# Kernel tuning notes

Measured on AMD Instinct MI355X. Metric: run time of the kernel, lower is better.

The kernel has to match this reference:

```python
import jax, jax.numpy as jnp
import numpy as np

N = 100000
NEG_SLOPE = 0.2
EPS = 1e-16


def _gatconv(h_in, src, dst, W, a_src, a_dst, b):
    # h_in: [N, Fin]; src/dst: [E_tot] (self-loops included); W: [Fin, Fout]
    h = h_in @ W                                  # [N, Fout]
    alpha_s = h @ a_src                           # [N]
    alpha_d = h @ a_dst                           # [N]
    e = alpha_s[src] + alpha_d[dst]               # [E_tot]
    e = jnp.where(e > 0, e, NEG_SLOPE * e)        # leaky_relu
    m = jax.ops.segment_max(e, dst, num_segments=N)
    e = jnp.exp(e - m[dst])
    s = jax.ops.segment_sum(e, dst, num_segments=N)
    alpha = e / (s[dst] + EPS)                    # segment softmax over in-edges of each dst
    out = jax.ops.segment_sum(alpha[:, None] * h[src], dst, num_segments=N)
    return out + b


def setup_inputs() -> dict:
    key = jax.random.key(0)
    ks = jax.random.split(key, 10)
    Fin, Fh, Fo = 64, 64, 40
    E = 1600000
    x = jax.random.normal(ks[0], (N, Fin), dtype=jnp.float32)
    edge_index = jax.random.randint(ks[1], (2, E), 0, N, dtype=jnp.int64)
    g = 1.0 / np.sqrt(Fin)
    W1 = jax.random.uniform(ks[2], (Fin, Fh), jnp.float32, -g, g)
    a_src1 = jax.random.uniform(ks[3], (Fh,), jnp.float32, -g, g)
    a_dst1 = jax.random.uniform(ks[4], (Fh,), jnp.float32, -g, g)
    b1 = jnp.zeros((Fh,), jnp.float32)
    g2 = 1.0 / np.sqrt(Fh)
    W2 = jax.random.uniform(ks[5], (Fh, Fo), jnp.float32, -g2, g2)
    a_src2 = jax.random.uniform(ks[6], (Fo,), jnp.float32, -g2, g2)
    a_dst2 = jax.random.uniform(ks[7], (Fo,), jnp.float32, -g2, g2)
    b2 = jnp.zeros((Fo,), jnp.float32)
    return {"x": x, "edge_index": edge_index, "W1": W1, "a_src1": a_src1,
            "a_dst1": a_dst1, "b1": b1, "W2": W2, "a_src2": a_src2,
            "a_dst2": a_dst2, "b2": b2}


def reference(x, edge_index, W1, a_src1, a_dst1, b1, W2, a_src2, a_dst2, b2):
    # add self loops (PyG GATConv default)
    loops = jnp.arange(N, dtype=edge_index.dtype)
    src = jnp.concatenate([edge_index[0], loops])
    dst = jnp.concatenate([edge_index[1], loops])
    h = _gatconv(x, src, dst, W1, a_src1, a_dst1, b1)
    h = jax.nn.relu(h)  # dropout p=0 / eval -> no-op
    h = _gatconv(h, src, dst, W2, a_src2, a_dst2, b2)
    return jax.nn.log_softmax(h, axis=-1)
```

## Files before the change

### kernel.cpp

```cpp
#include <hip/hip_runtime.h>
#include <math.h>

#ifndef NEG_SLOPE
#define NEG_SLOPE 0.2f
#endif

#define BUCK_BITS 9
#define BUCK_SIZE 512
#define BUCK_CAP  12288
#define PA_ILP    8

__global__ void detect_i64(const int* __restrict__ ei, int* __restrict__ flag) {
    int lane = threadIdx.x & 63;
    int bad = 0;
    for (int j = 0; j < 4; ++j) bad |= (ei[2 * (lane * 4 + j) + 1] != 0);
    unsigned long long m = __ballot(bad);
    if (lane == 0) *flag = (m == 0ull) ? 1 : 0;
}

__device__ __forceinline__ void get_edge(const void* ei, int is64, int e, int E,
                                         int& s, int& d) {
    if (e >= E) { s = e - E; d = s; return; }
    if (is64) {
        const long long* p = (const long long*)ei;
        s = (int)p[e];
        d = (int)p[(long long)E + e];
    } else {
        const int* p = (const int*)ei;
        s = p[e];
        d = p[E + e];
    }
}

__device__ __forceinline__ unsigned f2bf1(float x) {
    unsigned u = __float_as_uint(x);
    return (u + 0x7fffu + ((u >> 16) & 1u)) >> 16;
}

template <int F, int TPR>
__global__ __launch_bounds__(256) void gemm_att(
    const float* __restrict__ A, const float* __restrict__ W,
    const float* __restrict__ avs, const float* __restrict__ avd,
    unsigned short* __restrict__ Hb, float* __restrict__ as_out,
    float* __restrict__ ad_out, int Nrows) {
    constexpr int K = 64;
    constexpr int R = 256 / TPR;
    constexpr int C = F / TPR;
    __shared__ float sW[K * F];
    __shared__ float sA[R * (K + 4)];
    __shared__ float sas[F], sad[F];

    const int t = threadIdx.x;
    for (int i = t; i < K * F / 4; i += 256)
        ((float4*)sW)[i] = ((const float4*)W)[i];
    for (int i = t; i < F; i += 256) { sas[i] = avs[i]; sad[i] = avd[i]; }

    const int base = blockIdx.x * R;
    for (int i = t; i < R * (K / 4); i += 256) {
        int row = i >> 4;
        int c4  = i & 15;
        float4 v = make_float4(0.f, 0.f, 0.f, 0.f);
        if (base + row < Nrows)
            v = ((const float4*)(A + (size_t)(base + row) * K))[c4];
        float* dp = &sA[row * (K + 4) + c4 * 4];
        dp[0] = v.x; dp[1] = v.y; dp[2] = v.z; dp[3] = v.w;
    }
    __syncthreads();

    const int r  = t / TPR;
    const int f0 = (t % TPR) * C;
    float acc[C];
#pragma unroll
    for (int j = 0; j < C; ++j) acc[j] = 0.f;
    const float* sa = &sA[r * (K + 4)];
#pragma unroll
    for (int k = 0; k < K; ++k) {
        float av = sa[k];
        const float* w = &sW[k * F + f0];
#pragma unroll
        for (int j = 0; j < C; ++j) acc[j] += av * w[j];
    }

    float ps = 0.f, pd = 0.f;
#pragma unroll
    for (int j = 0; j < C; ++j) { ps += acc[j] * sas[f0 + j]; pd += acc[j] * sad[f0 + j]; }
#pragma unroll
    for (int off = 1; off < TPR; off <<= 1) {
        ps += __shfl_xor(ps, off);
        pd += __shfl_xor(pd, off);
    }

    const int row = base + r;
    if (row < Nrows) {
        if ((t % TPR) == 0) { as_out[row] = ps; ad_out[row] = pd; }
        unsigned* hp = (unsigned*)(Hb + (size_t)row * F + f0);
#pragma unroll
        for (int j = 0; j < C / 2; ++j)
            hp[j] = f2bf1(acc[2 * j]) | (f2bf1(acc[2 * j + 1]) << 16);
    }
}

__global__ __launch_bounds__(256) void bucket_bin(
    const void* __restrict__ ei, const int* __restrict__ flag,
    int* __restrict__ fill, int2* __restrict__ pairs, int E, int Etot) {
    __shared__ int cnt[256];
    __shared__ int goff[256];
    const int is64 = *flag;
    const int t = threadIdx.x;
    cnt[t] = 0;
    __syncthreads();
    const int base = blockIdx.x * (256 * PA_ILP) + t;
    int s[PA_ILP], d[PA_ILP], r[PA_ILP];
    bool ok[PA_ILP];
#pragma unroll
    for (int u = 0; u < PA_ILP; ++u) {
        int e = base + u * 256;
        ok[u] = (e < Etot);
        s[u] = d[u] = 0;
        if (ok[u]) get_edge(ei, is64, e, E, s[u], d[u]);
    }
#pragma unroll
    for (int u = 0; u < PA_ILP; ++u)
        if (ok[u]) r[u] = atomicAdd(&cnt[d[u] >> BUCK_BITS], 1);
    __syncthreads();
    if (cnt[t] > 0) goff[t] = atomicAdd(&fill[t], cnt[t]);
    __syncthreads();
#pragma unroll
    for (int u = 0; u < PA_ILP; ++u) {
        if (ok[u]) {
            int b = d[u] >> BUCK_BITS;
            int idx = goff[b] + r[u];
            if (idx < BUCK_CAP)
                pairs[(size_t)b * BUCK_CAP + idx] = make_int2(s[u], d[u]);
        }
    }
}

__global__ void bucket_scan(const int* __restrict__ fill, int* __restrict__ bases,
                            int* __restrict__ row_ptrN, int nbuck) {
    const int lane = threadIdx.x & 63;
    int v[4];
    int loc = 0;
#pragma unroll
    for (int i = 0; i < 4; ++i) {
        int idx = lane * 4 + i;
        v[i] = (idx < nbuck) ? fill[idx] : 0;
        loc += v[i];
    }
    int x = loc;
    for (int off = 1; off < 64; off <<= 1) {
        int y = __shfl_up(x, off);
        if (lane >= off) x += y;
    }
    int run = x - loc;
#pragma unroll
    for (int i = 0; i < 4; ++i) {
        int idx = lane * 4 + i;
        if (idx < nbuck) bases[idx] = run;
        run += v[i];
    }
    if (lane == 63) *row_ptrN = x;
}

__global__ __launch_bounds__(256) void bucket_csr(
    const int2* __restrict__ pairs, const int* __restrict__ fill,
    const int* __restrict__ bases, int* __restrict__ row_ptr,
    int* __restrict__ csr_src, int N) {
    __shared__ int cnt[BUCK_SIZE];
    __shared__ int offs[BUCK_SIZE];
    const int b = blockIdx.x;
    const int base_d = b << BUCK_BITS;
    const int t = threadIdx.x;
    int m = fill[b];
    if (m > BUCK_CAP) m = BUCK_CAP;
    const int gb = bases[b];
    cnt[t] = 0; cnt[t + 256] = 0;
    __syncthreads();
    const int2* bp = pairs + (size_t)b * BUCK_CAP;

    int i = t;
    for (; i + 768 < m; i += 1024) {
        int2 p0 = bp[i], p1 = bp[i + 256], p2 = bp[i + 512], p3 = bp[i + 768];
        atomicAdd(&cnt[p0.y - base_d], 1);
        atomicAdd(&cnt[p1.y - base_d], 1);
        atomicAdd(&cnt[p2.y - base_d], 1);
        atomicAdd(&cnt[p3.y - base_d], 1);
    }
    for (; i < m; i += 256) atomicAdd(&cnt[bp[i].y - base_d], 1);
    __syncthreads();

    if (t < 64) {
        int v[8];
        int loc = 0;
#pragma unroll
        for (int j = 0; j < 8; ++j) { v[j] = cnt[t * 8 + j]; loc += v[j]; }
        int x = loc;
        for (int off = 1; off < 64; off <<= 1) {
            int y = __shfl_up(x, off);
            if (t >= off) x += y;
        }
        int run = x - loc;
#pragma unroll
        for (int j = 0; j < 8; ++j) { offs[t * 8 + j] = gb + run; run += v[j]; }
    }
    __syncthreads();

    for (int k = t; k < BUCK_SIZE; k += 256) {
        int d = base_d + k;
        if (d < N) row_ptr[d] = offs[k];
    }
    __syncthreads();

    i = t;
    for (; i + 768 < m; i += 1024) {
        int2 p0 = bp[i], p1 = bp[i + 256], p2 = bp[i + 512], p3 = bp[i + 768];
        csr_src[atomicAdd(&offs[p0.y - base_d], 1)] = p0.x;
        csr_src[atomicAdd(&offs[p1.y - base_d], 1)] = p1.x;
        csr_src[atomicAdd(&offs[p2.y - base_d], 1)] = p2.x;
        csr_src[atomicAdd(&offs[p3.y - base_d], 1)] = p3.x;
    }
    for (; i < m; i += 256) {
        int2 p = bp[i];
        csr_src[atomicAdd(&offs[p.y - base_d], 1)] = p.x;
    }
}

__device__ __forceinline__ void bf16x8_fma(uint4 hv, float w, float* acc) {
    const unsigned* u = (const unsigned*)&hv;
#pragma unroll
    for (int i = 0; i < 4; ++i) {
        float lo = __uint_as_float(u[i] << 16);
        float hi = __uint_as_float(u[i] & 0xffff0000u);
        acc[2 * i]     += w * lo;
        acc[2 * i + 1] += w * hi;
    }
}

template <int F, int NC, bool RELU, bool LSM>
__global__ __launch_bounds__(256) void gat_aggregate4(
    const int* __restrict__ row_ptr, const int* __restrict__ csr_src,
    const float* __restrict__ asn, const float* __restrict__ adn,
    const unsigned short* __restrict__ Hb, const float* __restrict__ bias,
    float* __restrict__ out, int N) {
    const int lane    = threadIdx.x & 63;
    const int sub     = lane & 15;
    const int half    = sub >> 3;
    const int q       = sub & 7;
    const int grpbase = lane & 48;
    const int node    = blockIdx.x * 16 + (threadIdx.x >> 4);
    const bool valid  = node < N;
    const int nd      = valid ? node : N - 1;
    const int qc      = (q < NC) ? q : NC - 1;
    const float qmask = (q < NC) ? 1.f : 0.f;

    const int r0 = row_ptr[nd], r1 = row_ptr[nd + 1];
    const float add = adn[nd];

    float acc[8];
#pragma unroll
    for (int i = 0; i < 8; ++i) acc[i] = 0.f;
    float Ssum = 0.f;

    for (int base = r0; base < r1; base += 16) {
        int cnt = r1 - base;
        if (cnt > 16) cnt = 16;
        int s = 0;
        float w = 0.f;
        if (sub < cnt) {
            s = csr_src[base + sub];
            float v = asn[s] + add;
            v = v > 0.f ? v : NEG_SLOPE * v;
            w = __expf(v);
        }
        Ssum += w;
        for (int j = 0; j < cnt; j += 8) {
            int se[4]; float we[4]; uint4 hv[4];
#pragma unroll
            for (int k = 0; k < 4; ++k) {
                int e = j + 2 * k + half;
                int src_lane = grpbase | (e & 15);
                se[k] = __shfl(s, src_lane);
                float wk = __shfl(w, src_lane) * qmask;
                we[k] = (e < cnt) ? wk : 0.f;
            }
#pragma unroll
            for (int k = 0; k < 4; ++k)
                hv[k] = *(const uint4*)(Hb + (size_t)se[k] * F + qc * 8);
#pragma unroll
            for (int k = 0; k < 4; ++k) bf16x8_fma(hv[k], we[k], acc);
        }
    }
#pragma unroll
    for (int i = 0; i < 8; ++i) acc[i] += __shfl_xor(acc[i], 8);
#pragma unroll
    for (int off = 1; off < 16; off <<= 1) Ssum += __shfl_xor(Ssum, off);
    const float inv = 1.f / (Ssum + 1e-16f);
    float r[8];
#pragma unroll
    for (int i = 0; i < 8; ++i) r[i] = acc[i] * inv;

    if (LSM) {
        float val[8];
#pragma unroll
        for (int i = 0; i < 8; ++i) val[i] = r[i] + bias[qc * 8 + i];
        float mx = -3.0e38f;
        if (q < NC) {
#pragma unroll
            for (int i = 0; i < 8; ++i) mx = fmaxf(mx, val[i]);
        }
#pragma unroll
        for (int off = 1; off <= 4; off <<= 1) mx = fmaxf(mx, __shfl_xor(mx, off));
        float sm = 0.f;
        if (q < NC) {
#pragma unroll
            for (int i = 0; i < 8; ++i) sm += __expf(val[i] - mx);
        }
#pragma unroll
        for (int off = 1; off <= 4; off <<= 1) sm += __shfl_xor(sm, off);
        float ls = logf(sm) + mx;
        if (valid && half == 0 && q < NC) {
            float* op = out + (size_t)node * F + q * 8;
            ((float4*)op)[0] = make_float4(val[0] - ls, val[1] - ls, val[2] - ls, val[3] - ls);
            ((float4*)op)[1] = make_float4(val[4] - ls, val[5] - ls, val[6] - ls, val[7] - ls);
        }
    } else {
        if (valid && half == 0 && q < NC) {
            float* op = out + (size_t)node * F + q * 8;
            float4 o0, o1;
            o0.x = r[0] + bias[q * 8 + 0]; o0.y = r[1] + bias[q * 8 + 1];
            o0.z = r[2] + bias[q * 8 + 2]; o0.w = r[3] + bias[q * 8 + 3];
            o1.x = r[4] + bias[q * 8 + 4]; o1.y = r[5] + bias[q * 8 + 5];
            o1.z = r[6] + bias[q * 8 + 6]; o1.w = r[7] + bias[q * 8 + 7];
            if (RELU) {
                o0.x = fmaxf(o0.x, 0.f); o0.y = fmaxf(o0.y, 0.f);
                o0.z = fmaxf(o0.z, 0.f); o0.w = fmaxf(o0.w, 0.f);
                o1.x = fmaxf(o1.x, 0.f); o1.y = fmaxf(o1.y, 0.f);
                o1.z = fmaxf(o1.z, 0.f); o1.w = fmaxf(o1.w, 0.f);
            }
            ((float4*)op)[0] = o0;
            ((float4*)op)[1] = o1;
        }
    }
}

extern "C" void kernel_launch(void* const* d_in, const int* in_sizes, int n_in,
                              void* d_out, int out_size, void* d_ws, size_t ws_size,
                              hipStream_t stream) {
    const float* x   = (const float*)d_in[0];
    const void*  ei  = d_in[1];
    const float* W1  = (const float*)d_in[2];
    const float* as1 = (const float*)d_in[3];
    const float* ad1 = (const float*)d_in[4];
    const float* b1  = (const float*)d_in[5];
    const float* W2  = (const float*)d_in[6];
    const float* as2 = (const float*)d_in[7];
    const float* ad2 = (const float*)d_in[8];
    const float* b2  = (const float*)d_in[9];
    float* out = (float*)d_out;

    const int N     = in_sizes[0] / 64;
    const int E     = in_sizes[1] / 2;
    const int Etot  = E + N;
    const int nbuck = (N + BUCK_SIZE - 1) >> BUCK_BITS;

    float* ws = (float*)d_ws;
    unsigned short* hb = (unsigned short*)ws;  ws += (size_t)N * 32;
    float* agg1 = ws;              ws += (size_t)N * 64;
    float* asn  = ws;              ws += N;
    float* adn  = ws;              ws += N;
    int* row_ptr = (int*)ws;       ws += N + 1;
    int* csr_src = (int*)ws;       ws += Etot;
    int* fill   = (int*)ws;        ws += 256;
    int* bases  = (int*)ws;        ws += 256;
    int* flag   = (int*)ws;
    int2* pairs = (int2*)hb;

    detect_i64<<<1, 64, 0, stream>>>((const int*)ei, flag);

    hipMemsetAsync(fill, 0, 256 * sizeof(int), stream);
    {
        int pb = (Etot + 256 * PA_ILP - 1) / (256 * PA_ILP);
        bucket_bin<<<pb, 256, 0, stream>>>(ei, flag, fill, pairs, E, Etot);
    }
    bucket_scan<<<1, 64, 0, stream>>>(fill, bases, &row_ptr[N], nbuck);
    bucket_csr<<<nbuck, 256, 0, stream>>>(pairs, fill, bases, row_ptr, csr_src, N);

    const int AGG_B = (N + 15) / 16;

    gemm_att<64, 4><<<(N + 63) / 64, 256, 0, stream>>>(x, W1, as1, ad1, hb, asn, adn, N);
    gat_aggregate4<64, 8, true, false><<<AGG_B, 256, 0, stream>>>(
        row_ptr, csr_src, asn, adn, hb, b1, agg1, N);

    gemm_att<40, 4><<<(N + 63) / 64, 256, 0, stream>>>(agg1, W2, as2, ad2, hb, asn, adn, N);
    gat_aggregate4<40, 5, false, true><<<AGG_B, 256, 0, stream>>>(
        row_ptr, csr_src, asn, adn, hb, b2, out, N);
}
```

Before: 263.4 us.

## Fuse edge binning with layer-1 GEMM and layer-1 aggregation with layer-2 GEMM

Merges the i64 detection, edge bucketing and the first dense projection into one heterogeneous launch, with blocks split by index. The bucket prefix scan moves into each bucket_csr block. The layer-1 softmax aggregation is fused with the layer-2 projection and attention dot products, so the fp32 hidden activations are never written to or reread from global memory. This cuts launch count and a large intermediate round trip, at the cost of heavier shared-memory use, lower occupancy in the fused kernels, and a separate pairs buffer that enlarges the workspace.

```diff
diff --git a/kernel.cpp b/kernel.cpp
--- a/kernel.cpp
+++ b/kernel.cpp
@@ -9,14 +9,6 @@
 #define BUCK_SIZE 512
 #define BUCK_CAP  12288
 #define PA_ILP    8
-
-__global__ void detect_i64(const int* __restrict__ ei, int* __restrict__ flag) {
-    int lane = threadIdx.x & 63;
-    int bad = 0;
-    for (int j = 0; j < 4; ++j) bad |= (ei[2 * (lane * 4 + j) + 1] != 0);
-    unsigned long long m = __ballot(bad);
-    if (lane == 0) *flag = (m == 0ull) ? 1 : 0;
-}
 
 __device__ __forceinline__ void get_edge(const void* ei, int is64, int e, int E,
                                          int& s, int& d) {
@@ -37,145 +29,150 @@
     return (u + 0x7fffu + ((u >> 16) & 1u)) >> 16;
 }
 
-template <int F, int TPR>
-__global__ __launch_bounds__(256) void gemm_att(
-    const float* __restrict__ A, const float* __restrict__ W,
+__global__ __launch_bounds__(256) void bin_gemm1(
+    const void* __restrict__ ei, int E, int Etot, int binB,
+    int* __restrict__ fill, int2* __restrict__ pairs,
+    const float* __restrict__ x, const float* __restrict__ W1,
     const float* __restrict__ avs, const float* __restrict__ avd,
-    unsigned short* __restrict__ Hb, float* __restrict__ as_out,
-    float* __restrict__ ad_out, int Nrows) {
-    constexpr int K = 64;
-    constexpr int R = 256 / TPR;
-    constexpr int C = F / TPR;
-    __shared__ float sW[K * F];
-    __shared__ float sA[R * (K + 4)];
-    __shared__ float sas[F], sad[F];
-
+    unsigned short* __restrict__ Hb, float* __restrict__ asn,
+    float* __restrict__ adn, int N) {
+    __shared__ __align__(16) char smem[34816];
     const int t = threadIdx.x;
-    for (int i = t; i < K * F / 4; i += 256)
-        ((float4*)sW)[i] = ((const float4*)W)[i];
-    for (int i = t; i < F; i += 256) { sas[i] = avs[i]; sad[i] = avd[i]; }
-
-    const int base = blockIdx.x * R;
-    for (int i = t; i < R * (K / 4); i += 256) {
-        int row = i >> 4;
-        int c4  = i & 15;
-        float4 v = make_float4(0.f, 0.f, 0.f, 0.f);
-        if (base + row < Nrows)
-            v = ((const float4*)(A + (size_t)(base + row) * K))[c4];
-        float* dp = &sA[row * (K + 4) + c4 * 4];
-        dp[0] = v.x; dp[1] = v.y; dp[2] = v.z; dp[3] = v.w;
-    }
-    __syncthreads();
-
-    const int r  = t / TPR;
-    const int f0 = (t % TPR) * C;
-    float acc[C];
-#pragma unroll
-    for (int j = 0; j < C; ++j) acc[j] = 0.f;
-    const float* sa = &sA[r * (K + 4)];
-#pragma unroll
-    for (int k = 0; k < K; ++k) {
-        float av = sa[k];
-        const float* w = &sW[k * F + f0];
-#pragma unroll
-        for (int j = 0; j < C; ++j) acc[j] += av * w[j];
-    }
-
-    float ps = 0.f, pd = 0.f;
-#pragma unroll
-    for (int j = 0; j < C; ++j) { ps += acc[j] * sas[f0 + j]; pd += acc[j] * sad[f0 + j]; }
-#pragma unroll
-    for (int off = 1; off < TPR; off <<= 1) {
-        ps += __shfl_xor(ps, off);
-        pd += __shfl_xor(pd, off);
-    }
-
-    const int row = base + r;
-    if (row < Nrows) {
-        if ((t % TPR) == 0) { as_out[row] = ps; ad_out[row] = pd; }
-        unsigned* hp = (unsigned*)(Hb + (size_t)row * F + f0);
-#pragma unroll
-        for (int j = 0; j < C / 2; ++j)
-            hp[j] = f2bf1(acc[2 * j]) | (f2bf1(acc[2 * j + 1]) << 16);
-    }
-}
-
-__global__ __launch_bounds__(256) void bucket_bin(
-    const void* __restrict__ ei, const int* __restrict__ flag,
-    int* __restrict__ fill, int2* __restrict__ pairs, int E, int Etot) {
-    __shared__ int cnt[256];
-    __shared__ int goff[256];
-    const int is64 = *flag;
-    const int t = threadIdx.x;
-    cnt[t] = 0;
-    __syncthreads();
-    const int base = blockIdx.x * (256 * PA_ILP) + t;
-    int s[PA_ILP], d[PA_ILP], r[PA_ILP];
-    bool ok[PA_ILP];
-#pragma unroll
-    for (int u = 0; u < PA_ILP; ++u) {
-        int e = base + u * 256;
-        ok[u] = (e < Etot);
-        s[u] = d[u] = 0;
-        if (ok[u]) get_edge(ei, is64, e, E, s[u], d[u]);
-    }
-#pragma unroll
-    for (int u = 0; u < PA_ILP; ++u)
-        if (ok[u]) r[u] = atomicAdd(&cnt[d[u] >> BUCK_BITS], 1);
-    __syncthreads();
-    if (cnt[t] > 0) goff[t] = atomicAdd(&fill[t], cnt[t]);
-    __syncthreads();
-#pragma unroll
-    for (int u = 0; u < PA_ILP; ++u) {
-        if (ok[u]) {
-            int b = d[u] >> BUCK_BITS;
-            int idx = goff[b] + r[u];
-            if (idx < BUCK_CAP)
-                pairs[(size_t)b * BUCK_CAP + idx] = make_int2(s[u], d[u]);
-        }
-    }
-}
-
-__global__ void bucket_scan(const int* __restrict__ fill, int* __restrict__ bases,
-                            int* __restrict__ row_ptrN, int nbuck) {
-    const int lane = threadIdx.x & 63;
-    int v[4];
-    int loc = 0;
-#pragma unroll
-    for (int i = 0; i < 4; ++i) {
-        int idx = lane * 4 + i;
-        v[i] = (idx < nbuck) ? fill[idx] : 0;
-        loc += v[i];
-    }
-    int x = loc;
-    for (int off = 1; off < 64; off <<= 1) {
-        int y = __shfl_up(x, off);
-        if (lane >= off) x += y;
-    }
-    int run = x - loc;
-#pragma unroll
-    for (int i = 0; i < 4; ++i) {
-        int idx = lane * 4 + i;
-        if (idx < nbuck) bases[idx] = run;
-        run += v[i];
-    }
-    if (lane == 63) *row_ptrN = x;
+
+    if ((int)blockIdx.x < binB) {
+        int* cnt   = (int*)smem;
+        int* goff  = cnt + 256;
+        int* sflag = goff + 256;
+        if (t < 64) {
+            const int* p = (const int*)ei;
+            int bad = 0;
+            for (int j = 0; j < 4; ++j) bad |= (p[2 * (t * 4 + j) + 1] != 0);
+            unsigned long long m = __ballot(bad);
+            if (t == 0) *sflag = (m == 0ull) ? 1 : 0;
+        }
+        cnt[t] = 0;
+        __syncthreads();
+        const int is64 = *sflag;
+        const int base = blockIdx.x * (256 * PA_ILP) + t;
+        int s[PA_ILP], d[PA_ILP], r[PA_ILP];
+        bool ok[PA_ILP];
+#pragma unroll
+        for (int u = 0; u < PA_ILP; ++u) {
+            int e = base + u * 256;
+            ok[u] = (e < Etot);
+            s[u] = d[u] = 0;
+            if (ok[u]) get_edge(ei, is64, e, E, s[u], d[u]);
+        }
+#pragma unroll
+        for (int u = 0; u < PA_ILP; ++u)
+            if (ok[u]) r[u] = atomicAdd(&cnt[d[u] >> BUCK_BITS], 1);
+        __syncthreads();
+        if (cnt[t] > 0) goff[t] = atomicAdd(&fill[t], cnt[t]);
+        __syncthreads();
+#pragma unroll
+        for (int u = 0; u < PA_ILP; ++u) {
+            if (ok[u]) {
+                int b = d[u] >> BUCK_BITS;
+                int idx = goff[b] + r[u];
+                if (idx < BUCK_CAP)
+                    pairs[(size_t)b * BUCK_CAP + idx] = make_int2(s[u], d[u]);
+            }
+        }
+    } else {
+        constexpr int K = 64, F = 64, TPR = 4, R = 64, C = 16;
+        float* sW  = (float*)smem;
+        float* sA  = sW + K * F;
+        float* sas = sA + R * (K + 4);
+        float* sad = sas + F;
+
+        for (int i = t; i < K * F / 4; i += 256)
+            ((float4*)sW)[i] = ((const float4*)W1)[i];
+        for (int i = t; i < F; i += 256) { sas[i] = avs[i]; sad[i] = avd[i]; }
+
+        const int base = (blockIdx.x - binB) * R;
+        for (int i = t; i < R * (K / 4); i += 256) {
+            int row = i >> 4;
+            int c4  = i & 15;
+            float4 v = make_float4(0.f, 0.f, 0.f, 0.f);
+            if (base + row < N)
+                v = ((const float4*)(x + (size_t)(base + row) * K))[c4];
+            float* dp = &sA[row * (K + 4) + c4 * 4];
+            dp[0] = v.x; dp[1] = v.y; dp[2] = v.z; dp[3] = v.w;
+        }
+        __syncthreads();
+
+        const int r  = t / TPR;
+        const int f0 = (t % TPR) * C;
+        float acc[C];
+#pragma unroll
+        for (int j = 0; j < C; ++j) acc[j] = 0.f;
+        const float* sa = &sA[r * (K + 4)];
+#pragma unroll
+        for (int k = 0; k < K; ++k) {
+            float av = sa[k];
+            const float* w = &sW[k * F + f0];
+#pragma unroll
+            for (int j = 0; j < C; ++j) acc[j] += av * w[j];
+        }
+        float ps = 0.f, pd = 0.f;
+#pragma unroll
+        for (int j = 0; j < C; ++j) { ps += acc[j] * sas[f0 + j]; pd += acc[j] * sad[f0 + j]; }
+#pragma unroll
+        for (int off = 1; off < TPR; off <<= 1) {
+            ps += __shfl_xor(ps, off);
+            pd += __shfl_xor(pd, off);
+        }
+        const int row = base + r;
+        if (row < N) {
+            if ((t % TPR) == 0) { asn[row] = ps; adn[row] = pd; }
+            unsigned* hp = (unsigned*)(Hb + (size_t)row * F + f0);
+#pragma unroll
+            for (int j = 0; j < C / 2; ++j)
+                hp[j] = f2bf1(acc[2 * j]) | (f2bf1(acc[2 * j + 1]) << 16);
+        }
+    }
 }
 
 __global__ __launch_bounds__(256) void bucket_csr(
     const int2* __restrict__ pairs, const int* __restrict__ fill,
-    const int* __restrict__ bases, int* __restrict__ row_ptr,
-    int* __restrict__ csr_src, int N) {
+    int* __restrict__ row_ptr, int* __restrict__ csr_src, int N, int nbuck) {
     __shared__ int cnt[BUCK_SIZE];
     __shared__ int offs[BUCK_SIZE];
+    __shared__ int sbase[256];
+    __shared__ int stot;
+    const int t = threadIdx.x;
+    if (t < 64) {
+        int v[4];
+        int loc = 0;
+#pragma unroll
+        for (int i = 0; i < 4; ++i) {
+            int idx = t * 4 + i;
+            v[i] = (idx < nbuck) ? fill[idx] : 0;
+            loc += v[i];
+        }
+        int x = loc;
+        for (int off = 1; off < 64; off <<= 1) {
+            int y = __shfl_up(x, off);
+            if (t >= off) x += y;
+        }
+        int run = x - loc;
+#pragma unroll
+        for (int i = 0; i < 4; ++i) {
+            int idx = t * 4 + i;
+            if (idx < 256) sbase[idx] = run;
+            run += v[i];
+        }
+        if (t == 63) stot = x;
+    }
+    cnt[t] = 0; cnt[t + 256] = 0;
+    __syncthreads();
+
     const int b = blockIdx.x;
     const int base_d = b << BUCK_BITS;
-    const int t = threadIdx.x;
+    const int gb = sbase[b];
     int m = fill[b];
     if (m > BUCK_CAP) m = BUCK_CAP;
-    const int gb = bases[b];
-    cnt[t] = 0; cnt[t + 256] = 0;
-    __syncthreads();
+    if (b == 0 && t == 0) row_ptr[N] = stot;
     const int2* bp = pairs + (size_t)b * BUCK_CAP;
 
     int i = t;
@@ -236,12 +233,115 @@
     }
 }
 
-template <int F, int NC, bool RELU, bool LSM>
-__global__ __launch_bounds__(256) void gat_aggregate4(
+__global__ __launch_bounds__(256) void agg1_gemm2(
+    const int* __restrict__ row_ptr, const int* __restrict__ csr_src,
+    const float* __restrict__ asn1, const float* __restrict__ adn1,
+    const unsigned short* __restrict__ Hb, const float* __restrict__ b1,
+    const float* __restrict__ W2, const float* __restrict__ a_s2,
+    const float* __restrict__ a_d2, unsigned short* __restrict__ Hb2,
+    float* __restrict__ asn2, float* __restrict__ adn2, int N) {
+    __shared__ float sW2[64 * 40];
+    __shared__ float sa2[40], sd2[40], sb1[64];
+    __shared__ float rowbuf[16][68];
+    const int t = threadIdx.x;
+    for (int i = t; i < 640; i += 256) ((float4*)sW2)[i] = ((const float4*)W2)[i];
+    if (t < 40) { sa2[t] = a_s2[t]; sd2[t] = a_d2[t]; }
+    if (t >= 64 && t < 128) sb1[t - 64] = b1[t - 64];
+    __syncthreads();
+
+    const int lane    = t & 63;
+    const int sub     = lane & 15;
+    const int half    = sub >> 3;
+    const int q       = sub & 7;
+    const int grpbase = lane & 48;
+    const int slot    = t >> 4;
+    const int node    = blockIdx.x * 16 + slot;
+    const bool valid  = node < N;
+    const int nd      = valid ? node : N - 1;
+
+    const int r0 = row_ptr[nd], r1 = row_ptr[nd + 1];
+    const float add = adn1[nd];
+
+    float acc[8];
+#pragma unroll
+    for (int i = 0; i < 8; ++i) acc[i] = 0.f;
+    float Ssum = 0.f;
+
+    for (int base = r0; base < r1; base += 16) {
+        int cnt = r1 - base;
+        if (cnt > 16) cnt = 16;
+        int s = 0;
+        float w = 0.f;
+        if (sub < cnt) {
+            s = csr_src[base + sub];
+            float v = asn1[s] + add;
+            v = v > 0.f ? v : NEG_SLOPE * v;
+            w = __expf(v);
+        }
+        Ssum += w;
+        for (int j = 0; j < cnt; j += 8) {
+            int se[4]; float we[4]; uint4 hv[4];
+#pragma unroll
+            for (int k = 0; k < 4; ++k) {
+                int e = j + 2 * k + half;
+                int src_lane = grpbase | (e & 15);
+                se[k] = __shfl(s, src_lane);
+                float wk = __shfl(w, src_lane);
+                we[k] = (e < cnt) ? wk : 0.f;
+            }
+#pragma unroll
+            for (int k = 0; k < 4; ++k)
+                hv[k] = *(const uint4*)(Hb + (size_t)se[k] * 64 + q * 8);
+#pragma unroll
+            for (int k = 0; k < 4; ++k) bf16x8_fma(hv[k], we[k], acc);
+        }
+    }
+#pragma unroll
+    for (int i = 0; i < 8; ++i) acc[i] += __shfl_xor(acc[i], 8);
+#pragma unroll
+    for (int off = 1; off < 16; off <<= 1) Ssum += __shfl_xor(Ssum, off);
+    const float inv = 1.f / (Ssum + 1e-16f);
+
+    float row[8];
+#pragma unroll
+    for (int i = 0; i < 8; ++i) row[i] = fmaxf(acc[i] * inv + sb1[q * 8 + i], 0.f);
+    if (half == 0) {
+#pragma unroll
+        for (int i = 0; i < 8; ++i) rowbuf[slot][q * 8 + i] = row[i];
+    }
+
+    const bool m2 = (sub + 32) < 40;
+    const int f2c = m2 ? sub + 32 : 39;
+    float h2a = 0.f, h2b = 0.f, h2c = 0.f;
+#pragma unroll 8
+    for (int k = 0; k < 64; ++k) {
+        float a = rowbuf[slot][k];
+        h2a += a * sW2[k * 40 + sub];
+        h2b += a * sW2[k * 40 + sub + 16];
+        h2c += a * sW2[k * 40 + f2c];
+    }
+    float ps = h2a * sa2[sub] + h2b * sa2[sub + 16] + (m2 ? h2c * sa2[sub + 32] : 0.f);
+    float pd = h2a * sd2[sub] + h2b * sd2[sub + 16] + (m2 ? h2c * sd2[sub + 32] : 0.f);
+#pragma unroll
+    for (int off = 1; off < 16; off <<= 1) {
+        ps += __shfl_xor(ps, off);
+        pd += __shfl_xor(pd, off);
+    }
+    if (valid) {
+        unsigned short* hp = Hb2 + (size_t)node * 40;
+        hp[sub]      = (unsigned short)f2bf1(h2a);
+        hp[sub + 16] = (unsigned short)f2bf1(h2b);
+        if (m2) hp[sub + 32] = (unsigned short)f2bf1(h2c);
+        if (sub == 0) { asn2[node] = ps; adn2[node] = pd; }
+    }
+}
+
+__global__ __launch_bounds__(256) void agg2_lsm(
     const int* __restrict__ row_ptr, const int* __restrict__ csr_src,
     const float* __restrict__ asn, const float* __restrict__ adn,
     const unsigned short* __restrict__ Hb, const float* __restrict__ bias,
     float* __restrict__ out, int N) {
+    constexpr int F = 40, NC = 5;
     const int lane    = threadIdx.x & 63;
     const int sub     = lane & 15;
     const int half    = sub >> 3;
@@ -299,47 +399,28 @@
 #pragma unroll
     for (int i = 0; i < 8; ++i) r[i] = acc[i] * inv;
 
-    if (LSM) {
-        float val[8];
-#pragma unroll
-        for (int i = 0; i < 8; ++i) val[i] = r[i] + bias[qc * 8 + i];
-        float mx = -3.0e38f;
-        if (q < NC) {
-#pragma unroll
-            for (int i = 0; i < 8; ++i) mx = fmaxf(mx, val[i]);
-        }
-#pragma unroll
-        for (int off = 1; off <= 4; off <<= 1) mx = fmaxf(mx, __shfl_xor(mx, off));
-        float sm = 0.f;
-        if (q < NC) {
-#pragma unroll
-            for (int i = 0; i < 8; ++i) sm += __expf(val[i] - mx);
-        }
-#pragma unroll
-        for (int off = 1; off <= 4; off <<= 1) sm += __shfl_xor(sm, off);
-        float ls = logf(sm) + mx;
-        if (valid && half == 0 && q < NC) {
-            float* op = out + (size_t)node * F + q * 8;
-            ((float4*)op)[0] = make_float4(val[0] - ls, val[1] - ls, val[2] - ls, val[3] - ls);
-            ((float4*)op)[1] = make_float4(val[4] - ls, val[5] - ls, val[6] - ls, val[7] - ls);
-        }
-    } else {
-        if (valid && half == 0 && q < NC) {
-            float* op = out + (size_t)node * F + q * 8;
-            float4 o0, o1;
-            o0.x = r[0] + bias[q * 8 + 0]; o0.y = r[1] + bias[q * 8 + 1];
-            o0.z = r[2] + bias[q * 8 + 2]; o0.w = r[3] + bias[q * 8 + 3];
-            o1.x = r[4] + bias[q * 8 + 4]; o1.y = r[5] + bias[q * 8 + 5];
-            o1.z = r[6] + bias[q * 8 + 6]; o1.w = r[7] + bias[q * 8 + 7];
-            if (RELU) {
-                o0.x = fmaxf(o0.x, 0.f); o0.y = fmaxf(o0.y, 0.f);
-                o0.z = fmaxf(o0.z, 0.f); o0.w = fmaxf(o0.w, 0.f);
-                o1.x = fmaxf(o1.x, 0.f); o1.y = fmaxf(o1.y, 0.f);
-                o1.z = fmaxf(o1.z, 0.f); o1.w = fmaxf(o1.w, 0.f);
-            }
-            ((float4*)op)[0] = o0;
-            ((float4*)op)[1] = o1;
-        }
+    float val[8];
+#pragma unroll
+    for (int i = 0; i < 8; ++i) val[i] = r[i] + bias[qc * 8 + i];
+    float mx = -3.0e38f;
+    if (q < NC) {
+#pragma unroll
+        for (int i = 0; i < 8; ++i) mx = fmaxf(mx, val[i]);
+    }
+#pragma unroll
+    for (int off = 1; off <= 4; off <<= 1) mx = fmaxf(mx, __shfl_xor(mx, off));
+    float sm = 0.f;
+    if (q < NC) {
+#pragma unroll
+        for (int i = 0; i < 8; ++i) sm += __expf(val[i] - mx);
+    }
+#pragma unroll
+    for (int off = 1; off <= 4; off <<= 1) sm += __shfl_xor(sm, off);
+    float ls = logf(sm) + mx;
+    if (valid && half == 0 && q < NC) {
+        float* op = out + (size_t)node * F + q * 8;
+        ((float4*)op)[0] = make_float4(val[0] - ls, val[1] - ls, val[2] - ls, val[3] - ls);
+        ((float4*)op)[1] = make_float4(val[4] - ls, val[5] - ls, val[6] - ls, val[7] - ls);
     }
 }
 
@@ -364,34 +445,27 @@
     const int nbuck = (N + BUCK_SIZE - 1) >> BUCK_BITS;
 
     float* ws = (float*)d_ws;
-    unsigned short* hb = (unsigned short*)ws;  ws += (size_t)N * 32;
-    float* agg1 = ws;              ws += (size_t)N * 64;
-    float* asn  = ws;              ws += N;
-    float* adn  = ws;              ws += N;
+    unsigned short* hb  = (unsigned short*)ws;  ws += (size_t)N * 32;
+    unsigned short* hb2 = (unsigned short*)ws;  ws += (size_t)N * 20;
+    float* asn1 = ws;              ws += N;
+    float* adn1 = ws;              ws += N;
+    float* asn2 = ws;              ws += N;
+    float* adn2 = ws;              ws += N;
     int* row_ptr = (int*)ws;       ws += N + 1;
     int* csr_src = (int*)ws;       ws += Etot;
     int* fill   = (int*)ws;        ws += 256;
-    int* bases  = (int*)ws;        ws += 256;
-    int* flag   = (int*)ws;
-    int2* pairs = (int2*)hb;
-
-    detect_i64<<<1, 64, 0, stream>>>((const int*)ei, flag);
+    int2* pairs = (int2*)ws;       ws += (size_t)256 * BUCK_CAP * 2;
+
+    const int binB  = (Etot + 256 * PA_ILP - 1) / (256 * PA_ILP);
+    const int gemmB = (N + 63) / 64;
+    const int AGG_B = (N + 15) / 16;
 
     hipMemsetAsync(fill, 0, 256 * sizeof(int), stream);
-    {
-        int pb = (Etot + 256 * PA_ILP - 1) / (256 * PA_ILP);
-        bucket_bin<<<pb, 256, 0, stream>>>(ei, flag, fill, pairs, E, Etot);
-    }
-    bucket_scan<<<1, 64, 0, stream>>>(fill, bases, &row_ptr[N], nbuck);
-    bucket_csr<<<nbuck, 256, 0, stream>>>(pairs, fill, bases, row_ptr, csr_src, N);
-
-    const int AGG_B = (N + 15) / 16;
-
-    gemm_att<64, 4><<<(N + 63) / 64, 256, 0, stream>>>(x, W1, as1, ad1, hb, asn, adn, N);
-    gat_aggregate4<64, 8, true, false><<<AGG_B, 256, 0, stream>>>(
-        row_ptr, csr_src, asn, adn, hb, b1, agg1, N);
-
-    gemm_att<40, 4><<<(N + 63) / 64, 256, 0, stream>>>(agg1, W2, as2, ad2, hb, asn, adn, N);
-    gat_aggregate4<40, 5, false, true><<<AGG_B, 256, 0, stream>>>(
-        row_ptr, csr_src, asn, adn, hb, b2, out, N);
-}
+    bin_gemm1<<<binB + gemmB, 256, 0, stream>>>(
+        ei, E, Etot, binB, fill, pairs, x, W1, as1, ad1, hb, asn1, adn1, N);
+    bucket_csr<<<nbuck, 256, 0, stream>>>(pairs, fill, row_ptr, csr_src, N, nbuck);
+    agg1_gemm2<<<AGG_B, 256, 0, stream>>>(
+        row_ptr, csr_src, asn1, adn1, hb, b1, W2, as2, ad2, hb2, asn2, adn2, N);
+    agg2_lsm<<<AGG_B, 256, 0, stream>>>(
+        row_ptr, csr_src, asn2, adn2, hb2, b2, out, N);
+}
```

Result: faster. 246.8 us (-6.3%).
